# Kernel optimization log

Measured on AMD Instinct MI355X. Metric: run time of the kernel, lower is better.

The kernel has to match this reference:

```python
import jax, jax.numpy as jnp
import numpy as np


def setup_inputs() -> dict:
    key = jax.random.key(0)
    k1, k2 = jax.random.split(key)
    B, H, W, D, K = 32, 64, 64, 64, 512
    inputs = jax.random.normal(k1, (B, H, W, D), dtype=jnp.float32)
    # codebook: (D, K) as in the keras layer (embedding_dim x num_embeddings)
    embeddings = jax.random.uniform(k2, (D, K), dtype=jnp.float32,
                                    minval=-1.0, maxval=1.0) * (3.0 / D) ** 0.5
    return {"inputs": inputs, "embeddings": embeddings}


def reference(inputs, embeddings):
    # inputs: [B, H, W, D]; embeddings: [D, K]
    D = inputs.shape[-1]
    flat = inputs.reshape(-1, D)                                   # [N, D]
    distances = (jnp.sum(flat * flat, axis=1, keepdims=True)
                 - 2.0 * (flat @ embeddings)
                 + jnp.sum(embeddings * embeddings, axis=0, keepdims=True))
    encoding_indices = jnp.argmin(distances, axis=1)               # [N]
    encoding_indices = encoding_indices.reshape(inputs.shape[:-1])  # [B, H, W]
    quantized = jnp.take(embeddings.T, encoding_indices, axis=0)   # [B, H, W, D]
    # straight-through estimator
    return inputs + jax.lax.stop_gradient(quantized - inputs)
```

## Files before the change

### kernel.cpp

```cpp
#include <hip/hip_runtime.h>


#define KC 512
#define DD 64
#define TAU 5e-4f

typedef __attribute__((ext_vector_type(8))) short short8;
typedef __attribute__((ext_vector_type(4))) float float4v;

__device__ inline unsigned short f2bf(float f) {
    unsigned u = __float_as_uint(f);
    return (unsigned short)((u + 0x7FFF + ((u >> 16) & 1)) >> 16);
}
__device__ inline float bf2f(unsigned short b) {
    return __uint_as_float((unsigned)b << 16);
}

__global__ __launch_bounds__(256) void vq_prep(const float* __restrict__ emb,
                                               float* __restrict__ et,
                                               float* __restrict__ bias,
                                               short* __restrict__ Bh,
                                               short* __restrict__ Bl) {
    __shared__ float tile[DD][17];
    const int ct = blockIdx.x;
    const int t  = threadIdx.x;

    {
        const int d = t >> 2, c0 = (t & 3) * 4;
        float4 v = *(const float4*)(emb + (size_t)d * KC + ct * 16 + c0);
        tile[d][c0 + 0] = v.x; tile[d][c0 + 1] = v.y;
        tile[d][c0 + 2] = v.z; tile[d][c0 + 3] = v.w;
    }
    __syncthreads();

    if (t < 16) {
        float s = 0.f;
        #pragma unroll
        for (int d = 0; d < DD; ++d) { float v = tile[d][t]; s += v * v; }
        bias[ct * 16 + t] = s;
    }

    {
        const int c = t >> 4, d0 = (t & 15) * 4;
        float4 v;
        v.x = tile[d0 + 0][c]; v.y = tile[d0 + 1][c];
        v.z = tile[d0 + 2][c]; v.w = tile[d0 + 3][c];
        *(float4*)(et + (size_t)(ct * 16 + c) * DD + d0) = v;
    }

    {
        const int term = t >> 7;
        const int kc   = (t >> 6) & 1;
        const int l    = t & 63;
        const int c    = l & 15, dq = l >> 4;
        short v8[8];
        #pragma unroll
        for (int j = 0; j < 8; ++j) {
            float f = tile[kc * 32 + dq * 8 + j][c];
            unsigned short h = f2bf(f);
            v8[j] = (short)(term == 0 ? h : f2bf(f - bf2f(h)));
        }
        short* dst = (term == 0 ? Bh : Bl) + ((size_t)(ct * 2 + kc) * 64 + l) * 8;
        *(short8*)dst = *(short8*)v8;
    }
}

__global__ __launch_bounds__(256) void vq_main(const float* __restrict__ x_in,
                                               const short* __restrict__ Bh,
                                               const short* __restrict__ Bl,
                                               const float* __restrict__ bias,
                                               const float* __restrict__ et,
                                               float* __restrict__ out) {
    __shared__ float bias_s[KC];
    __shared__ int   k1s[128];
    __shared__ float gaps[128];

    const int t = threadIdx.x, w = t >> 6, l = t & 63;
    const int col = l & 15, quad = l >> 4;
    const int R0 = blockIdx.x * 128;

    {
        float2 b2 = *(const float2*)(bias + 2 * t);
        bias_s[2 * t + 0] = b2.x; bias_s[2 * t + 1] = b2.y;
    }

    short8 ah[2][2], al[2][2];
    #pragma unroll
    for (int rt = 0; rt < 2; ++rt)
        #pragma unroll
        for (int kc = 0; kc < 2; ++kc) {
            const float* xp = x_in + (size_t)(R0 + w * 32 + rt * 16 + col) * DD
                            + kc * 32 + quad * 8;
            float4 xa = *(const float4*)xp;
            float4 xb = *(const float4*)(xp + 4);
            float f[8] = {xa.x, xa.y, xa.z, xa.w, xb.x, xb.y, xb.z, xb.w};
            #pragma unroll
            for (int j = 0; j < 8; ++j) {
                unsigned short h = f2bf(f[j]);
                ah[rt][kc][j] = (short)h;
                al[rt][kc][j] = (short)f2bf(f[j] - bf2f(h));
            }
        }
    __syncthreads();

    float v1[2][4], v2[2][4];
    int   k1[2][4];
    #pragma unroll
    for (int rt = 0; rt < 2; ++rt)
        #pragma unroll
        for (int r = 0; r < 4; ++r) {
            v1[rt][r] = 3.4e38f; v2[rt][r] = 3.4e38f; k1[rt][r] = 0;
        }

    #pragma unroll 2
    for (int ct = 0; ct < 32; ++ct) {
        short8 bh0 = *(const short8*)(Bh + ((size_t)(ct * 2 + 0) * 64 + l) * 8);
        short8 bh1 = *(const short8*)(Bh + ((size_t)(ct * 2 + 1) * 64 + l) * 8);
        short8 bl0 = *(const short8*)(Bl + ((size_t)(ct * 2 + 0) * 64 + l) * 8);
        short8 bl1 = *(const short8*)(Bl + ((size_t)(ct * 2 + 1) * 64 + l) * 8);
        float bs = bias_s[ct * 16 + col];
        const int kk = ct * 16 + col;
        #pragma unroll
        for (int rt = 0; rt < 2; ++rt) {
            float4v c = {0.f, 0.f, 0.f, 0.f};
            c = __builtin_amdgcn_mfma_f32_16x16x32_bf16(ah[rt][0], bh0, c, 0, 0, 0);
            c = __builtin_amdgcn_mfma_f32_16x16x32_bf16(ah[rt][1], bh1, c, 0, 0, 0);
            c = __builtin_amdgcn_mfma_f32_16x16x32_bf16(al[rt][0], bh0, c, 0, 0, 0);
            c = __builtin_amdgcn_mfma_f32_16x16x32_bf16(al[rt][1], bh1, c, 0, 0, 0);
            c = __builtin_amdgcn_mfma_f32_16x16x32_bf16(ah[rt][0], bl0, c, 0, 0, 0);
            c = __builtin_amdgcn_mfma_f32_16x16x32_bf16(ah[rt][1], bl1, c, 0, 0, 0);
            #pragma unroll
            for (int r = 0; r < 4; ++r) {
                float s = fmaf(c[r], -2.0f, bs);
                bool lt = s < v1[rt][r];
                v2[rt][r] = lt ? v1[rt][r] : fminf(v2[rt][r], s);
                k1[rt][r] = lt ? kk : k1[rt][r];
                v1[rt][r] = lt ? s : v1[rt][r];
            }
        }
    }

    #pragma unroll
    for (int rt = 0; rt < 2; ++rt)
        #pragma unroll
        for (int r = 0; r < 4; ++r) {
            float bv1 = v1[rt][r], bv2 = v2[rt][r];
            int   bk  = k1[rt][r];
            #pragma unroll
            for (int m = 1; m <= 8; m <<= 1) {
                float ov1 = __shfl_xor(bv1, m, 64);
                float ov2 = __shfl_xor(bv2, m, 64);
                int   ok  = __shfl_xor(bk,  m, 64);
                float nv2 = fminf(fminf(bv2, ov2), fmaxf(bv1, ov1));
                bool take = (ov1 < bv1) || (ov1 == bv1 && ok < bk);
                bv1 = take ? ov1 : bv1;
                bk  = take ? ok  : bk;
                bv2 = nv2;
            }
            if (col == 0) {
                int row_l = w * 32 + rt * 16 + quad * 4 + r;
                k1s[row_l]  = bk;
                gaps[row_l] = bv2 - bv1;
            }
        }

    for (int rr = 0; rr < 32; ++rr) {
        const int row_l = w * 32 + rr;
        if (gaps[row_l] <= TAU) {
            const size_t grow = (size_t)(R0 + row_l) * DD;
            const int kbase = l * 8;
            float acc[8];
            #pragma unroll
            for (int j = 0; j < 8; ++j) acc[j] = 0.f;
            for (int d0 = 0; d0 < DD; d0 += 4) {
                float4 xv = *(const float4*)(x_in + grow + d0);
                #pragma unroll
                for (int j = 0; j < 8; ++j) {
                    float4 ev = *(const float4*)(et + (size_t)(kbase + j) * DD + d0);
                    acc[j] += xv.x * ev.x;
                    acc[j] += xv.y * ev.y;
                    acc[j] += xv.z * ev.z;
                    acc[j] += xv.w * ev.w;
                }
            }
            float4 b0 = *(const float4*)(bias + kbase);
            float4 b1 = *(const float4*)(bias + kbase + 4);
            float bb[8] = {b0.x, b0.y, b0.z, b0.w, b1.x, b1.y, b1.z, b1.w};
            float bv = 3.4e38f; int bk = 0;
            #pragma unroll
            for (int j = 0; j < 8; ++j) {
                float s = bb[j] - 2.f * acc[j];
                if (s < bv) { bv = s; bk = kbase + j; }
            }
            #pragma unroll
            for (int m = 1; m <= 32; m <<= 1) {
                float ov = __shfl_xor(bv, m, 64);
                int   ok = __shfl_xor(bk, m, 64);
                if (ov < bv || (ov == bv && ok < bk)) { bv = ov; bk = ok; }
            }
            if (l == 0) k1s[row_l] = bk;
        }
    }
    __syncthreads();

    {
        const int row_l = t >> 1, half = t & 1;
        const int bk = k1s[row_l];
        const float4* qp = (const float4*)(et + (size_t)bk * DD + half * 32);
        float4* op = (float4*)(out + (size_t)(R0 + row_l) * DD + half * 32);
        #pragma unroll
        for (int i = 0; i < 8; ++i) op[i] = qp[i];
    }
}

extern "C" void kernel_launch(void* const* d_in, const int* in_sizes, int n_in,
                              void* d_out, int out_size, void* d_ws, size_t ws_size,
                              hipStream_t stream) {
    const float* x_in = (const float*)d_in[0];
    const float* emb  = (const float*)d_in[1];
    float* out = (float*)d_out;

    float* et   = (float*)d_ws;
    float* bias = et + KC * DD;
    short* Bh   = (short*)(bias + KC);
    short* Bl   = Bh + 32 * 2 * 64 * 8;

    const int N = out_size / DD;

    vq_prep<<<32, 256, 0, stream>>>(emb, et, bias, Bh, Bl);
    vq_main<<<N / 128, 256, 0, stream>>>(x_in, Bh, Bl, bias, et, out);
}
```

Before: 134.6 us.

## Keep codebook slices in registers per wave and stream input rows through LDS

```diff
diff --git a/kernel.cpp b/kernel.cpp
--- a/kernel.cpp
+++ b/kernel.cpp
@@ -4,6 +4,7 @@
 #define KC 512
 #define DD 64
 #define TAU 5e-4f
+#define HTAU (0.5f * TAU)
 
 typedef __attribute__((ext_vector_type(8))) short short8;
 typedef __attribute__((ext_vector_type(4))) float float4v;
@@ -65,108 +66,174 @@
     }
 }
 
-__global__ __launch_bounds__(256) void vq_main(const float* __restrict__ x_in,
-                                               const short* __restrict__ Bh,
-                                               const short* __restrict__ Bl,
-                                               const float* __restrict__ bias,
-                                               const float* __restrict__ et,
-                                               float* __restrict__ out) {
-    __shared__ float bias_s[KC];
-    __shared__ int   k1s[128];
-    __shared__ float gaps[128];
+__global__ __launch_bounds__(256, 2) void vq_main(const float* __restrict__ x_in,
+                                                  const short* __restrict__ Bh,
+                                                  const short* __restrict__ Bl,
+                                                  const float* __restrict__ bias,
+                                                  const float* __restrict__ et,
+                                                  float* __restrict__ out) {
+    __shared__ __align__(16) short A_lds[2][8][512];
+    __shared__ float pv1[4][256];
+    __shared__ float pv2[4][256];
+    __shared__ int   pkk[4][256];
+    __shared__ int   k1s[256];
+    __shared__ float gaps[256];
 
     const int t = threadIdx.x, w = t >> 6, l = t & 63;
     const int col = l & 15, quad = l >> 4;
-    const int R0 = blockIdx.x * 128;
-
-    {
-        float2 b2 = *(const float2*)(bias + 2 * t);
-        bias_s[2 * t + 0] = b2.x; bias_s[2 * t + 1] = b2.y;
-    }
-
-    short8 ah[2][2], al[2][2];
+    const int R0 = blockIdx.x * 256;
+
+    short8 BH[8][2], BL[8][2];
     #pragma unroll
-    for (int rt = 0; rt < 2; ++rt)
+    for (int cl = 0; cl < 8; ++cl)
         #pragma unroll
         for (int kc = 0; kc < 2; ++kc) {
-            const float* xp = x_in + (size_t)(R0 + w * 32 + rt * 16 + col) * DD
-                            + kc * 32 + quad * 8;
-            float4 xa = *(const float4*)xp;
-            float4 xb = *(const float4*)(xp + 4);
-            float f[8] = {xa.x, xa.y, xa.z, xa.w, xb.x, xb.y, xb.z, xb.w};
+            BH[cl][kc] = *(const short8*)(Bh + ((size_t)((w * 8 + cl) * 2 + kc) * 64 + l) * 8);
+            BL[cl][kc] = *(const short8*)(Bl + ((size_t)((w * 8 + cl) * 2 + kc) * 64 + l) * 8);
+        }
+    float bhalf[8];
+    #pragma unroll
+    for (int cl = 0; cl < 8; ++cl)
+        bhalf[cl] = -0.5f * bias[(w * 8 + cl) * 16 + col];
+
+    const int s_row = (w >> 1) * 16 + col;
+    const int s_d   = (w & 1) * 32 + quad * 8;
+    const int fh = w * 2, flo = w * 2 + 1;
+
+    {
+        const float* p = x_in + (size_t)(R0 + s_row) * DD + s_d;
+        float4 xa = *(const float4*)p;
+        float4 xb = *(const float4*)(p + 4);
+        float f[8] = {xa.x, xa.y, xa.z, xa.w, xb.x, xb.y, xb.z, xb.w};
+        short8 hi8, lo8;
+        #pragma unroll
+        for (int j = 0; j < 8; ++j) {
+            unsigned short h = f2bf(f[j]);
+            hi8[j] = (short)h;
+            lo8[j] = (short)f2bf(f[j] - bf2f(h));
+        }
+        *(short8*)&A_lds[0][fh][l * 8]  = hi8;
+        *(short8*)&A_lds[0][flo][l * 8] = lo8;
+    }
+    __syncthreads();
+
+    #pragma unroll 1
+    for (int tt = 0; tt < 8; ++tt) {
+        const int cur = tt & 1;
+
+        float4 nxa, nxb;
+        if (tt < 7) {
+            const float* p = x_in + (size_t)(R0 + (tt + 1) * 32 + s_row) * DD + s_d;
+            nxa = *(const float4*)p;
+            nxb = *(const float4*)(p + 4);
+        }
+
+        short8 ah[2][2], al[2][2];
+        #pragma unroll
+        for (int rt = 0; rt < 2; ++rt)
+            #pragma unroll
+            for (int kc = 0; kc < 2; ++kc) {
+                ah[rt][kc] = *(const short8*)&A_lds[cur][(rt * 2 + kc) * 2 + 0][l * 8];
+                al[rt][kc] = *(const short8*)&A_lds[cur][(rt * 2 + kc) * 2 + 1][l * 8];
+            }
+
+        float m1[2][4], m2[2][4];
+        int   kb[2][4];
+        #pragma unroll
+        for (int rt = 0; rt < 2; ++rt)
+            #pragma unroll
+            for (int r = 0; r < 4; ++r) {
+                m1[rt][r] = -3.4e38f; m2[rt][r] = -3.4e38f; kb[rt][r] = 0;
+            }
+
+        #pragma unroll
+        for (int cl = 0; cl < 8; ++cl) {
+            const int kk = (w * 8 + cl) * 16 + col;
+            #pragma unroll
+            for (int rt = 0; rt < 2; ++rt) {
+                float4v c = {bhalf[cl], bhalf[cl], bhalf[cl], bhalf[cl]};
+                c = __builtin_amdgcn_mfma_f32_16x16x32_bf16(ah[rt][0], BH[cl][0], c, 0, 0, 0);
+                c = __builtin_amdgcn_mfma_f32_16x16x32_bf16(ah[rt][1], BH[cl][1], c, 0, 0, 0);
+                c = __builtin_amdgcn_mfma_f32_16x16x32_bf16(al[rt][0], BH[cl][0], c, 0, 0, 0);
+                c = __builtin_amdgcn_mfma_f32_16x16x32_bf16(al[rt][1], BH[cl][1], c, 0, 0, 0);
+                c = __builtin_amdgcn_mfma_f32_16x16x32_bf16(ah[rt][0], BL[cl][0], c, 0, 0, 0);
+                c = __builtin_amdgcn_mfma_f32_16x16x32_bf16(ah[rt][1], BL[cl][1], c, 0, 0, 0);
+                #pragma unroll
+                for (int r = 0; r < 4; ++r) {
+                    bool gt = c[r] > m1[rt][r];
+                    m2[rt][r] = fmaxf(fminf(c[r], m1[rt][r]), m2[rt][r]);
+                    kb[rt][r] = gt ? kk : kb[rt][r];
+                    m1[rt][r] = gt ? c[r] : m1[rt][r];
+                }
+            }
+        }
+
+        #pragma unroll
+        for (int rt = 0; rt < 2; ++rt)
+            #pragma unroll
+            for (int r = 0; r < 4; ++r) {
+                float b1 = m1[rt][r], b2 = m2[rt][r];
+                int   bk = kb[rt][r];
+                #pragma unroll
+                for (int m = 1; m <= 8; m <<= 1) {
+                    float o1 = __shfl_xor(b1, m, 64);
+                    float o2 = __shfl_xor(b2, m, 64);
+                    int   ok = __shfl_xor(bk, m, 64);
+                    float n2 = fmaxf(fmaxf(b2, o2), fminf(b1, o1));
+                    bool take = (o1 > b1) || (o1 == b1 && ok < bk);
+                    b1 = take ? o1 : b1;
+                    bk = take ? ok : bk;
+                    b2 = n2;
+                }
+                if (col == 0) {
+                    const int rowg = tt * 32 + rt * 16 + quad * 4 + r;
+                    pv1[w][rowg] = b1;
+                    pv2[w][rowg] = b2;
+                    pkk[w][rowg] = bk;
+                }
+            }
+
+        if (tt < 7) {
+            float f[8] = {nxa.x, nxa.y, nxa.z, nxa.w, nxb.x, nxb.y, nxb.z, nxb.w};
+            short8 hi8, lo8;
             #pragma unroll
             for (int j = 0; j < 8; ++j) {
                 unsigned short h = f2bf(f[j]);
-                ah[rt][kc][j] = (short)h;
-                al[rt][kc][j] = (short)f2bf(f[j] - bf2f(h));
-            }
-        }
-    __syncthreads();
-
-    float v1[2][4], v2[2][4];
-    int   k1[2][4];
-    #pragma unroll
-    for (int rt = 0; rt < 2; ++rt)
-        #pragma unroll
-        for (int r = 0; r < 4; ++r) {
-            v1[rt][r] = 3.4e38f; v2[rt][r] = 3.4e38f; k1[rt][r] = 0;
-        }
-
-    #pragma unroll 2
-    for (int ct = 0; ct < 32; ++ct) {
-        short8 bh0 = *(const short8*)(Bh + ((size_t)(ct * 2 + 0) * 64 + l) * 8);
-        short8 bh1 = *(const short8*)(Bh + ((size_t)(ct * 2 + 1) * 64 + l) * 8);
-        short8 bl0 = *(const short8*)(Bl + ((size_t)(ct * 2 + 0) * 64 + l) * 8);
-        short8 bl1 = *(const short8*)(Bl + ((size_t)(ct * 2 + 1) * 64 + l) * 8);
-        float bs = bias_s[ct * 16 + col];
-        const int kk = ct * 16 + col;
-        #pragma unroll
-        for (int rt = 0; rt < 2; ++rt) {
-            float4v c = {0.f, 0.f, 0.f, 0.f};
-            c = __builtin_amdgcn_mfma_f32_16x16x32_bf16(ah[rt][0], bh0, c, 0, 0, 0);
-            c = __builtin_amdgcn_mfma_f32_16x16x32_bf16(ah[rt][1], bh1, c, 0, 0, 0);
-            c = __builtin_amdgcn_mfma_f32_16x16x32_bf16(al[rt][0], bh0, c, 0, 0, 0);
-            c = __builtin_amdgcn_mfma_f32_16x16x32_bf16(al[rt][1], bh1, c, 0, 0, 0);
-            c = __builtin_amdgcn_mfma_f32_16x16x32_bf16(ah[rt][0], bl0, c, 0, 0, 0);
-            c = __builtin_amdgcn_mfma_f32_16x16x32_bf16(ah[rt][1], bl1, c, 0, 0, 0);
-            #pragma unroll
-            for (int r = 0; r < 4; ++r) {
-                float s = fmaf(c[r], -2.0f, bs);
-                bool lt = s < v1[rt][r];
-                v2[rt][r] = lt ? v1[rt][r] : fminf(v2[rt][r], s);
-                k1[rt][r] = lt ? kk : k1[rt][r];
-                v1[rt][r] = lt ? s : v1[rt][r];
-            }
-        }
-    }
-
-    #pragma unroll
-    for (int rt = 0; rt < 2; ++rt)
-        #pragma unroll
-        for (int r = 0; r < 4; ++r) {
-            float bv1 = v1[rt][r], bv2 = v2[rt][r];
-            int   bk  = k1[rt][r];
-            #pragma unroll
-            for (int m = 1; m <= 8; m <<= 1) {
-                float ov1 = __shfl_xor(bv1, m, 64);
-                float ov2 = __shfl_xor(bv2, m, 64);
-                int   ok  = __shfl_xor(bk,  m, 64);
-                float nv2 = fminf(fminf(bv2, ov2), fmaxf(bv1, ov1));
-                bool take = (ov1 < bv1) || (ov1 == bv1 && ok < bk);
-                bv1 = take ? ov1 : bv1;
-                bk  = take ? ok  : bk;
-                bv2 = nv2;
-            }
-            if (col == 0) {
-                int row_l = w * 32 + rt * 16 + quad * 4 + r;
-                k1s[row_l]  = bk;
-                gaps[row_l] = bv2 - bv1;
-            }
-        }
-
-    for (int rr = 0; rr < 32; ++rr) {
-        const int row_l = w * 32 + rr;
-        if (gaps[row_l] <= TAU) {
+                hi8[j] = (short)h;
+                lo8[j] = (short)f2bf(f[j] - bf2f(h));
+            }
+            __syncthreads();
+            *(short8*)&A_lds[cur ^ 1][fh][l * 8]  = hi8;
+            *(short8*)&A_lds[cur ^ 1][flo][l * 8] = lo8;
+            __syncthreads();
+        }
+    }
+    __syncthreads();
+
+    {
+        float b1 = pv1[0][t], b2 = pv2[0][t];
+        int   bk = pkk[0][t];
+        #pragma unroll
+        for (int wv = 1; wv < 4; ++wv) {
+            float v1 = pv1[wv][t], v2 = pv2[wv][t];
+            int   vk = pkk[wv][t];
+            bool gt = v1 > b1;
+            float nb2 = gt ? fmaxf(b1, v2) : fmaxf(b2, v1);
+            bk = gt ? vk : bk;
+            b1 = gt ? v1 : b1;
+            b2 = nb2;
+        }
+        k1s[t]  = bk;
+        gaps[t] = b1 - b2;
+    }
+    __syncthreads();
+
+    {
+        unsigned long long mask = __ballot(gaps[w * 64 + l] <= HTAU);
+        while (mask) {
+            const int rr = __builtin_ctzll(mask);
+            mask &= mask - 1;
+            const int row_l = w * 64 + rr;
             const size_t grow = (size_t)(R0 + row_l) * DD;
             const int kbase = l * 8;
             float acc[8];
@@ -184,8 +251,8 @@
                 }
             }
             float4 b0 = *(const float4*)(bias + kbase);
-            float4 b1 = *(const float4*)(bias + kbase + 4);
-            float bb[8] = {b0.x, b0.y, b0.z, b0.w, b1.x, b1.y, b1.z, b1.w};
+            float4 b1v = *(const float4*)(bias + kbase + 4);
+            float bb[8] = {b0.x, b0.y, b0.z, b0.w, b1v.x, b1v.y, b1v.z, b1v.w};
             float bv = 3.4e38f; int bk = 0;
             #pragma unroll
             for (int j = 0; j < 8; ++j) {
@@ -204,12 +271,15 @@
     __syncthreads();
 
     {
-        const int row_l = t >> 1, half = t & 1;
-        const int bk = k1s[row_l];
-        const float4* qp = (const float4*)(et + (size_t)bk * DD + half * 32);
-        float4* op = (float4*)(out + (size_t)(R0 + row_l) * DD + half * 32);
-        #pragma unroll
-        for (int i = 0; i < 8; ++i) op[i] = qp[i];
+        const int c4 = (t & 15) * 4;
+        const int rg = t >> 4;
+        #pragma unroll
+        for (int i = 0; i < 16; ++i) {
+            const int row = i * 16 + rg;
+            const int bk = k1s[row];
+            float4 v = *(const float4*)(et + (size_t)bk * DD + c4);
+            *(float4*)(out + (size_t)(R0 + row) * DD + c4) = v;
+        }
     }
 }
 
@@ -228,5 +298,5 @@
     const int N = out_size / DD;
 
     vq_prep<<<32, 256, 0, stream>>>(emb, et, bias, Bh, Bl);
-    vq_main<<<N / 128, 256, 0, stream>>>(x_in, Bh, Bl, bias, et, out);
-}
+    vq_main<<<N / 256, 256, 0, stream>>>(x_in, Bh, Bl, bias, et, out);
+}
```

New measurement: 168.4 us. 1.25x slower.

## Stage codebook in LDS, enlarge row tiles, fold bias into MFMA accumulator

Applied to the files above, without the earlier changes.

```diff
diff --git a/kernel.cpp b/kernel.cpp
--- a/kernel.cpp
+++ b/kernel.cpp
@@ -4,6 +4,7 @@
 #define KC 512
 #define DD 64
 #define TAU 5e-4f
+#define HTAU (0.5f * TAU)
 
 typedef __attribute__((ext_vector_type(8))) short short8;
 typedef __attribute__((ext_vector_type(4))) float float4v;
@@ -65,109 +66,127 @@
     }
 }
 
-__global__ __launch_bounds__(256) void vq_main(const float* __restrict__ x_in,
-                                               const short* __restrict__ Bh,
-                                               const short* __restrict__ Bl,
-                                               const float* __restrict__ bias,
-                                               const float* __restrict__ et,
-                                               float* __restrict__ out) {
+__global__ __launch_bounds__(512, 2) void vq_main(const float* __restrict__ x_in,
+                                                  const short* __restrict__ Bh,
+                                                  const short* __restrict__ Bl,
+                                                  const float* __restrict__ bias,
+                                                  const float* __restrict__ et,
+                                                  float* __restrict__ out) {
+    __shared__ __align__(16) short Bh_lds[32 * 2 * 64 * 8];
+    __shared__ __align__(16) short Bl_lds[32 * 2 * 64 * 8];
     __shared__ float bias_s[KC];
-    __shared__ int   k1s[128];
-    __shared__ float gaps[128];
+    __shared__ int   k1s[8][64];
+    __shared__ float gaps[8][64];
 
     const int t = threadIdx.x, w = t >> 6, l = t & 63;
     const int col = l & 15, quad = l >> 4;
-    const int R0 = blockIdx.x * 128;
-
-    {
-        float2 b2 = *(const float2*)(bias + 2 * t);
-        bias_s[2 * t + 0] = b2.x; bias_s[2 * t + 1] = b2.y;
-    }
-
-    short8 ah[2][2], al[2][2];
+    const int R0 = blockIdx.x * 512;
+    const int wrow0 = w * 64;
+
+    {
+        const float4* srcH = (const float4*)Bh;
+        const float4* srcL = (const float4*)Bl;
+        float4* dstH = (float4*)Bh_lds;
+        float4* dstL = (float4*)Bl_lds;
+        #pragma unroll
+        for (int j = 0; j < 8; ++j) {
+            const int idx = t + j * 512;
+            dstH[idx] = srcH[idx];
+            dstL[idx] = srcL[idx];
+        }
+        bias_s[t] = bias[t];
+    }
+
+    short8 AH[4][2], AL[4][2];
     #pragma unroll
-    for (int rt = 0; rt < 2; ++rt)
+    for (int rt = 0; rt < 4; ++rt)
         #pragma unroll
         for (int kc = 0; kc < 2; ++kc) {
-            const float* xp = x_in + (size_t)(R0 + w * 32 + rt * 16 + col) * DD
-                            + kc * 32 + quad * 8;
-            float4 xa = *(const float4*)xp;
-            float4 xb = *(const float4*)(xp + 4);
+            const float* p = x_in + (size_t)(R0 + wrow0 + rt * 16 + col) * DD
+                           + kc * 32 + quad * 8;
+            float4 xa = *(const float4*)p;
+            float4 xb = *(const float4*)(p + 4);
             float f[8] = {xa.x, xa.y, xa.z, xa.w, xb.x, xb.y, xb.z, xb.w};
+            short8 hi8, lo8;
             #pragma unroll
             for (int j = 0; j < 8; ++j) {
                 unsigned short h = f2bf(f[j]);
-                ah[rt][kc][j] = (short)h;
-                al[rt][kc][j] = (short)f2bf(f[j] - bf2f(h));
-            }
+                hi8[j] = (short)h;
+                lo8[j] = (short)f2bf(f[j] - bf2f(h));
+            }
+            AH[rt][kc] = hi8;
+            AL[rt][kc] = lo8;
         }
     __syncthreads();
 
-    float v1[2][4], v2[2][4];
-    int   k1[2][4];
+    float m1[4][4], m2[4][4];
+    int   kb[4][4];
     #pragma unroll
-    for (int rt = 0; rt < 2; ++rt)
+    for (int rt = 0; rt < 4; ++rt)
         #pragma unroll
         for (int r = 0; r < 4; ++r) {
-            v1[rt][r] = 3.4e38f; v2[rt][r] = 3.4e38f; k1[rt][r] = 0;
+            m1[rt][r] = -3.4e38f; m2[rt][r] = -3.4e38f; kb[rt][r] = 0;
         }
 
     #pragma unroll 2
     for (int ct = 0; ct < 32; ++ct) {
-        short8 bh0 = *(const short8*)(Bh + ((size_t)(ct * 2 + 0) * 64 + l) * 8);
-        short8 bh1 = *(const short8*)(Bh + ((size_t)(ct * 2 + 1) * 64 + l) * 8);
-        short8 bl0 = *(const short8*)(Bl + ((size_t)(ct * 2 + 0) * 64 + l) * 8);
-        short8 bl1 = *(const short8*)(Bl + ((size_t)(ct * 2 + 1) * 64 + l) * 8);
-        float bs = bias_s[ct * 16 + col];
+        short8 bh0 = *(const short8*)&Bh_lds[((ct * 2 + 0) * 64 + l) * 8];
+        short8 bh1 = *(const short8*)&Bh_lds[((ct * 2 + 1) * 64 + l) * 8];
+        short8 bl0 = *(const short8*)&Bl_lds[((ct * 2 + 0) * 64 + l) * 8];
+        short8 bl1 = *(const short8*)&Bl_lds[((ct * 2 + 1) * 64 + l) * 8];
+        const float ci = -0.5f * bias_s[ct * 16 + col];
         const int kk = ct * 16 + col;
         #pragma unroll
-        for (int rt = 0; rt < 2; ++rt) {
-            float4v c = {0.f, 0.f, 0.f, 0.f};
-            c = __builtin_amdgcn_mfma_f32_16x16x32_bf16(ah[rt][0], bh0, c, 0, 0, 0);
-            c = __builtin_amdgcn_mfma_f32_16x16x32_bf16(ah[rt][1], bh1, c, 0, 0, 0);
-            c = __builtin_amdgcn_mfma_f32_16x16x32_bf16(al[rt][0], bh0, c, 0, 0, 0);
-            c = __builtin_amdgcn_mfma_f32_16x16x32_bf16(al[rt][1], bh1, c, 0, 0, 0);
-            c = __builtin_amdgcn_mfma_f32_16x16x32_bf16(ah[rt][0], bl0, c, 0, 0, 0);
-            c = __builtin_amdgcn_mfma_f32_16x16x32_bf16(ah[rt][1], bl1, c, 0, 0, 0);
+        for (int rt = 0; rt < 4; ++rt) {
+            float4v c = {ci, ci, ci, ci};
+            c = __builtin_amdgcn_mfma_f32_16x16x32_bf16(AH[rt][0], bh0, c, 0, 0, 0);
+            c = __builtin_amdgcn_mfma_f32_16x16x32_bf16(AH[rt][1], bh1, c, 0, 0, 0);
+            c = __builtin_amdgcn_mfma_f32_16x16x32_bf16(AL[rt][0], bh0, c, 0, 0, 0);
+            c = __builtin_amdgcn_mfma_f32_16x16x32_bf16(AL[rt][1], bh1, c, 0, 0, 0);
+            c = __builtin_amdgcn_mfma_f32_16x16x32_bf16(AH[rt][0], bl0, c, 0, 0, 0);
+            c = __builtin_amdgcn_mfma_f32_16x16x32_bf16(AH[rt][1], bl1, c, 0, 0, 0);
             #pragma unroll
             for (int r = 0; r < 4; ++r) {
-                float s = fmaf(c[r], -2.0f, bs);
-                bool lt = s < v1[rt][r];
-                v2[rt][r] = lt ? v1[rt][r] : fminf(v2[rt][r], s);
-                k1[rt][r] = lt ? kk : k1[rt][r];
-                v1[rt][r] = lt ? s : v1[rt][r];
+                float cr = c[r];
+                bool gt = cr > m1[rt][r];
+                m2[rt][r] = fmaxf(fminf(cr, m1[rt][r]), m2[rt][r]);
+                kb[rt][r] = gt ? kk : kb[rt][r];
+                m1[rt][r] = fmaxf(m1[rt][r], cr);
             }
         }
     }
 
     #pragma unroll
-    for (int rt = 0; rt < 2; ++rt)
+    for (int rt = 0; rt < 4; ++rt)
         #pragma unroll
         for (int r = 0; r < 4; ++r) {
-            float bv1 = v1[rt][r], bv2 = v2[rt][r];
-            int   bk  = k1[rt][r];
+            float b1 = m1[rt][r], b2 = m2[rt][r];
+            int   bk = kb[rt][r];
             #pragma unroll
             for (int m = 1; m <= 8; m <<= 1) {
-                float ov1 = __shfl_xor(bv1, m, 64);
-                float ov2 = __shfl_xor(bv2, m, 64);
-                int   ok  = __shfl_xor(bk,  m, 64);
-                float nv2 = fminf(fminf(bv2, ov2), fmaxf(bv1, ov1));
-                bool take = (ov1 < bv1) || (ov1 == bv1 && ok < bk);
-                bv1 = take ? ov1 : bv1;
-                bk  = take ? ok  : bk;
-                bv2 = nv2;
+                float o1 = __shfl_xor(b1, m, 64);
+                float o2 = __shfl_xor(b2, m, 64);
+                int   ok = __shfl_xor(bk, m, 64);
+                float n2 = fmaxf(fmaxf(b2, o2), fminf(b1, o1));
+                bool take = (o1 > b1) || (o1 == b1 && ok < bk);
+                b1 = take ? o1 : b1;
+                bk = take ? ok : bk;
+                b2 = n2;
             }
             if (col == 0) {
-                int row_l = w * 32 + rt * 16 + quad * 4 + r;
-                k1s[row_l]  = bk;
-                gaps[row_l] = bv2 - bv1;
-            }
-        }
-
-    for (int rr = 0; rr < 32; ++rr) {
-        const int row_l = w * 32 + rr;
-        if (gaps[row_l] <= TAU) {
-            const size_t grow = (size_t)(R0 + row_l) * DD;
+                const int rowl = rt * 16 + quad * 4 + r;
+                k1s[w][rowl]  = bk;
+                gaps[w][rowl] = b1 - b2;
+            }
+        }
+    __syncthreads();
+
+    {
+        unsigned long long mask = __ballot(gaps[w][l] <= HTAU);
+        while (mask) {
+            const int rr = __builtin_ctzll(mask);
+            mask &= mask - 1;
+            const size_t grow = (size_t)(R0 + wrow0 + rr) * DD;
             const int kbase = l * 8;
             float acc[8];
             #pragma unroll
@@ -184,8 +203,8 @@
                 }
             }
             float4 b0 = *(const float4*)(bias + kbase);
-            float4 b1 = *(const float4*)(bias + kbase + 4);
-            float bb[8] = {b0.x, b0.y, b0.z, b0.w, b1.x, b1.y, b1.z, b1.w};
+            float4 b1v = *(const float4*)(bias + kbase + 4);
+            float bb[8] = {b0.x, b0.y, b0.z, b0.w, b1v.x, b1v.y, b1v.z, b1v.w};
             float bv = 3.4e38f; int bk = 0;
             #pragma unroll
             for (int j = 0; j < 8; ++j) {
@@ -198,18 +217,19 @@
                 int   ok = __shfl_xor(bk, m, 64);
                 if (ov < bv || (ov == bv && ok < bk)) { bv = ov; bk = ok; }
             }
-            if (l == 0) k1s[row_l] = bk;
-        }
-    }
-    __syncthreads();
-
-    {
-        const int row_l = t >> 1, half = t & 1;
-        const int bk = k1s[row_l];
-        const float4* qp = (const float4*)(et + (size_t)bk * DD + half * 32);
-        float4* op = (float4*)(out + (size_t)(R0 + row_l) * DD + half * 32);
-        #pragma unroll
-        for (int i = 0; i < 8; ++i) op[i] = qp[i];
+            if (l == 0) k1s[w][rr] = bk;
+        }
+    }
+
+    {
+        const int c4 = col * 4;
+        #pragma unroll
+        for (int i = 0; i < 16; ++i) {
+            const int rowl = i * 4 + quad;
+            const int bk = k1s[w][rowl];
+            float4 v = *(const float4*)(et + (size_t)bk * DD + c4);
+            *(float4*)(out + (size_t)(R0 + wrow0 + rowl) * DD + c4) = v;
+        }
     }
 }
 
@@ -228,5 +248,5 @@
     const int N = out_size / DD;
 
     vq_prep<<<32, 256, 0, stream>>>(emb, et, bias, Bh, Bl);
-    vq_main<<<N / 128, 256, 0, stream>>>(x_in, Bh, Bl, bias, et, out);
-}
+    vq_main<<<N / 512, 512, 0, stream>>>(x_in, Bh, Bl, bias, et, out);
+}
```

Measured after the change: 126.7 us. 5.9% less time.
